# Kernel tuning notes

Hardware: AMD Instinct MI355X
Metric: run time of the kernel (lower is better)

## Reference

```python
import jax, jax.numpy as jnp
import numpy as np

B, S, H, STEPS = 4096, 169, 64, 24  # batch, input seq (window 168 + covariate row), hidden, rollout steps


def _lstm(xseq, Wih, Whh, bih, bhh, h0, c0):
    """PyTorch-style single-layer LSTM. xseq: [B,T,D] -> ([B,T,H], hT, cT). Gate order i,f,g,o."""
    xg = jnp.einsum('btd,gd->btg', xseq, Wih) + (bih + bhh)  # precompute input proj [B,T,4H]

    def step(carry, xg_t):
        h, c = carry
        g = xg_t + h @ Whh.T
        i, f, gg, o = jnp.split(g, 4, axis=-1)
        c = jax.nn.sigmoid(f) * c + jax.nn.sigmoid(i) * jnp.tanh(gg)
        h = jax.nn.sigmoid(o) * jnp.tanh(c)
        return (h, c), h

    (hT, cT), hs = jax.lax.scan(step, (h0, c0), jnp.swapaxes(xg, 0, 1))
    return jnp.swapaxes(hs, 0, 1), hT, cT


def reference(x, Wih1, Whh1, bih1, bhh1, Wih2, Whh2, bih2, bhh2, fc1_w, fc1_b, fc2_w, fc2_b):
    win, d = x[:, :-1, :], x[:, -1, :]  # [B,168,1], [B,1]
    z = jnp.zeros((x.shape[0], H), x.dtype)

    def outer(win, _):
        h1s, h1, c1 = _lstm(win, Wih1, Whh1, bih1, bhh1, z, z)
        h1s = jax.nn.relu(h1s)
        # lstm2 is seeded with lstm1's final (h, c) state, as in the torch code
        h2s, _, _ = _lstm(h1s, Wih2, Whh2, bih2, bhh2, h1, c1)
        feat = jnp.concatenate([jax.nn.relu(h2s[:, -1, :]), d], axis=1)  # [B,65]
        out = (feat @ fc1_w.T + fc1_b) @ fc2_w.T + fc2_b  # [B,1] (no relu between fc1/fc2)
        win = jnp.concatenate([win[:, 1:, :], out[:, :, None]], axis=1)  # slide window
        return win, out[:, 0]

    _, outs = jax.lax.scan(outer, win, None, length=STEPS)  # outs: [24,B]
    return jnp.swapaxes(outs, 0, 1)  # [B,24]


def setup_inputs() -> dict:
    key = jax.random.key(0)
    ks = jax.random.split(key, 14)
    bnd = 1.0 / np.sqrt(H)

    def u(k, shape):
        return jax.random.uniform(k, shape, jnp.float32, -bnd, bnd)

    return {
        'x': jax.random.normal(ks[0], (B, S, 1), jnp.float32),
        'Wih1': u(ks[1], (4 * H, 1)),
        'Whh1': u(ks[2], (4 * H, H)),
        'bih1': u(ks[3], (4 * H,)),
        'bhh1': u(ks[4], (4 * H,)),
        'Wih2': u(ks[5], (4 * H, H)),
        'Whh2': u(ks[6], (4 * H, H)),
        'bih2': u(ks[7], (4 * H,)),
        'bhh2': u(ks[8], (4 * H,)),
        'fc1_w': u(ks[9], (64, 65)),
        'fc1_b': u(ks[10], (64,)),
        'fc2_w': u(ks[11], (1, 64)),
        'fc2_b': u(ks[12], (1,)),
    }
```

## Files before the change

kernel.cpp:

```cpp
#include <hip/hip_runtime.h>
#include <stdint.h>

#define NB 16
#define WIN 168
#define NSTEPS 24
#define NBLK (4096/NB)

typedef __attribute__((ext_vector_type(8))) short bf16x8;
typedef __attribute__((ext_vector_type(4))) float f32x4;

#if __has_builtin(__builtin_amdgcn_rcpf)
#define RCPF(x) __builtin_amdgcn_rcpf(x)
#else
#define RCPF(x) (1.0f / (x))
#endif
#if __has_builtin(__builtin_amdgcn_exp2f)
#define EXP2F(x) __builtin_amdgcn_exp2f(x)
#else
#define EXP2F(x) __expf((x) * 0.6931471805599453f)
#endif

__device__ __forceinline__ float sigm(float x){
  return RCPF(1.0f + EXP2F(x * -1.4426950408889634f));
}
__device__ __forceinline__ float tanh_(float x){
  return __builtin_fmaf(2.0f, RCPF(1.0f + EXP2F(x * -2.8853900817779268f)), -1.0f);
}

__device__ __forceinline__ uint32_t bf_rn(float f){
  uint32_t u = __builtin_bit_cast(uint32_t, f);
  return (u + 0x7FFFu + ((u >> 16) & 1u)) >> 16;
}
__device__ __forceinline__ float bf_f(uint32_t s){
  return __builtin_bit_cast(float, s << 16);
}
__device__ __forceinline__ void split_t(float f, uint32_t& hi, uint32_t& lo){
  uint32_t u = __builtin_bit_cast(uint32_t, f);
  hi = u >> 16;
  lo = bf_rn(f - bf_f(hi));
}
__device__ __forceinline__ void split_s(float f, short& hi, short& lo){
  uint32_t h = bf_rn(f);
  hi = (short)h;
  lo = (short)bf_rn(f - bf_f(h));
}
__device__ __forceinline__ f32x4 mfma16(bf16x8 a, bf16x8 b, f32x4 c){
  return __builtin_amdgcn_mfma_f32_16x16x32_bf16(a, b, c, 0, 0, 0);
}

__device__ __forceinline__ void lstm_epi(const f32x4 acc[4], float c[4], float hn[4]){
  #pragma unroll
  for (int r = 0; r < 4; r++){
    float gi = acc[0][r], gf = acc[1][r], gg = acc[2][r], go = acc[3][r];
    float cn = __builtin_fmaf(sigm(gf), c[r], sigm(gi) * tanh_(gg));
    c[r] = cn;
    hn[r] = sigm(go) * tanh_(cn);
  }
}

#define FROW 136
#define FBLK 544
#define FB(buf,hl,kt) ((((buf)*2 + (hl))*2 + (kt)) * FBLK)
#define BUF_INTS (2*FBLK)

template<bool USE_WS>
__global__ __launch_bounds__(256, 1) void lstm_rec_kernel(
  const float* __restrict__ x,    const float* __restrict__ Wih1, const float* __restrict__ Whh1,
  const float* __restrict__ bih1, const float* __restrict__ bhh1,
  const float* __restrict__ Wih2, const float* __restrict__ Whh2,
  const float* __restrict__ bih2, const float* __restrict__ bhh2,
  const float* __restrict__ fc1w, const float* __restrict__ fc1b,
  const float* __restrict__ fc2w, const float* __restrict__ fc2b,
  float* __restrict__ out, short* __restrict__ hist)
{
  __shared__ __align__(16) short h1f[2*2*2*FBLK];
  __shared__ __align__(16) short r1f[USE_WS ? 16 : 2*2*2*FBLK];
  __shared__ __align__(16) short rlf[USE_WS ? 16 : 2*2*2*FBLK];
  __shared__ float win_s[WIN][NB];
  __shared__ float Hlast[NB][68];
  __shared__ float fc1w_s[64*68];
  __shared__ float dval_s[NB];

  const int tid = threadIdx.x;
  const int wv  = tid >> 6;
  const int ln  = tid & 63;
  const int q   = ln >> 4;
  const int n   = ln & 15;
  const int bg0 = blockIdx.x * NB;
  const int u0  = 16*wv + 4*q;
  const int kt_  = u0 >> 5;
  const int q2_  = (u0 >> 3) & 3;
  const int jj0_ = u0 & 7;
  const int rdo  = q*FROW + n*8;
  const int wro  = q2_*FROW + n*8 + jj0_;
  const int gwo  = kt_*512 + q2_*128 + n*8 + jj0_;
  short* __restrict__ hblk = USE_WS ? (hist + (size_t)blockIdx.x * WIN * 2048) : nullptr;

  for (int i = tid; i < WIN*NB; i += 256){ int t = i >> 4, b = i & 15; win_s[t][b] = x[(bg0 + b)*169 + t]; }
  for (int i = tid; i < 64*65; i += 256){ int j = i / 65, k = i % 65; fc1w_s[j*68 + k] = fc1w[i]; }
  if (tid < NB) dval_s[tid] = x[(bg0 + tid)*169 + 168];

  const float fc1b_r = fc1b[ln];
  const float fc2w_r = fc2w[ln];
  const float fc2b_r = fc2b[0];

  bf16x8 A1hi[4][2], A1lo[4][2], Ain1[4];
  bf16x8 A2hi[4][4], A2lo[4][4];
  f32x4 b1c[4], b2c[4];
  #pragma unroll
  for (int e = 0; e < 4; e++){
    const int ja = 64*e + 16*wv + n;
    #pragma unroll
    for (int kt = 0; kt < 2; kt++){
      const float* p = Whh1 + ja*64 + kt*32 + q*8;
      #pragma unroll
      for (int jj = 0; jj < 8; jj++){ short h,l; split_s(p[jj], h, l); A1hi[e][kt][jj] = h; A1lo[e][kt][jj] = l; }
    }
    #pragma unroll
    for (int kt = 0; kt < 4; kt++){
      const float* p = (kt < 2 ? (Wih2 + ja*64 + kt*32) : (Whh2 + ja*64 + (kt-2)*32)) + q*8;
      #pragma unroll
      for (int jj = 0; jj < 8; jj++){ short h,l; split_s(p[jj], h, l); A2hi[e][kt][jj] = h; A2lo[e][kt][jj] = l; }
    }
    bf16x8 ain = {0,0,0,0,0,0,0,0};
    if (q == 0){ short wh, wl; split_s(Wih1[ja], wh, wl); ain[0] = wh; ain[1] = wh; ain[2] = wl; }
    Ain1[e] = ain;
    const int jc = 64*e + u0;
    #pragma unroll
    for (int r = 0; r < 4; r++){
      b1c[e][r] = bih1[jc+r] + bhh1[jc+r];
      b2c[e][r] = bih2[jc+r] + bhh2[jc+r];
    }
  }

  float c1[4], c2[4], c1r[4];

  auto lstm1_step = [&](short* S, float* cst, int rb, int wb, int slot, int relu_dst, int t){
    bf16x8 Bh0 = *(const bf16x8*)&S[FB(rb,0,0)+rdo];
    bf16x8 Bl0 = *(const bf16x8*)&S[FB(rb,1,0)+rdo];
    bf16x8 Bh1 = *(const bf16x8*)&S[FB(rb,0,1)+rdo];
    bf16x8 Bl1 = *(const bf16x8*)&S[FB(rb,1,1)+rdo];
    bf16x8 bin = {0,0,0,0,0,0,0,0};
    { float xv = win_s[slot][n]; uint32_t xh, xl; split_t(xv, xh, xl);
      if (q == 0){ bin[0] = (short)xh; bin[1] = (short)xl; bin[2] = (short)xh; } }
    f32x4 acc[4];
    #pragma unroll
    for (int e = 0; e < 4; e++){
      f32x4 a = b1c[e];
      a = mfma16(A1hi[e][0], Bh0, a);
      a = mfma16(A1hi[e][0], Bl0, a);
      a = mfma16(A1lo[e][0], Bh0, a);
      a = mfma16(A1hi[e][1], Bh1, a);
      a = mfma16(A1hi[e][1], Bl1, a);
      a = mfma16(A1lo[e][1], Bh1, a);
      a = mfma16(Ain1[e], bin, a);
      acc[e] = a;
    }
    float hn[4];
    lstm_epi(acc, cst, hn);
    uint32_t ph[4], pl[4];
    #pragma unroll
    for (int r = 0; r < 4; r++) split_t(hn[r], ph[r], pl[r]);
    *(uint2*)&S[FB(wb,0,kt_)+wro] = make_uint2(ph[0] | (ph[1]<<16), ph[2] | (ph[3]<<16));
    *(uint2*)&S[FB(wb,1,kt_)+wro] = make_uint2(pl[0] | (pl[1]<<16), pl[2] | (pl[3]<<16));
    if (relu_dst){
      uint32_t sh[4], sl[4];
      #pragma unroll
      for (int r = 0; r < 4; r++){ bool pos = hn[r] > 0.0f; sh[r] = pos ? ph[r] : 0u; sl[r] = pos ? pl[r] : 0u; }
      uint2 phi = make_uint2(sh[0] | (sh[1]<<16), sh[2] | (sh[3]<<16));
      uint2 plo = make_uint2(sl[0] | (sl[1]<<16), sl[2] | (sl[3]<<16));
      if (relu_dst == 1){
        short* Hp = hblk + (size_t)t * 2048;
        *(uint2*)&Hp[gwo]        = phi;
        *(uint2*)&Hp[1024 + gwo] = plo;
      } else {
        *(uint2*)&rlf[FB(rb,0,kt_)+wro] = phi;
        *(uint2*)&rlf[FB(rb,1,kt_)+wro] = plo;
      }
    }
  };

  auto lstm2_core = [&](bf16x8 L1h0, bf16x8 L1l0, bf16x8 L1h1, bf16x8 L1l1, int rbuf, int wbuf, bool last){
    bf16x8 L2h0 = *(const bf16x8*)&h1f[FB(rbuf,0,0)+rdo];
    bf16x8 L2l0 = *(const bf16x8*)&h1f[FB(rbuf,1,0)+rdo];
    bf16x8 L2h1 = *(const bf16x8*)&h1f[FB(rbuf,0,1)+rdo];
    bf16x8 L2l1 = *(const bf16x8*)&h1f[FB(rbuf,1,1)+rdo];
    f32x4 acc[4];
    #pragma unroll
    for (int e = 0; e < 4; e++){
      f32x4 a = b2c[e];
      a = mfma16(A2hi[e][0], L1h0, a);
      a = mfma16(A2hi[e][0], L1l0, a);
      a = mfma16(A2lo[e][0], L1h0, a);
      a = mfma16(A2hi[e][1], L1h1, a);
      a = mfma16(A2hi[e][1], L1l1, a);
      a = mfma16(A2lo[e][1], L1h1, a);
      a = mfma16(A2hi[e][2], L2h0, a);
      a = mfma16(A2hi[e][2], L2l0, a);
      a = mfma16(A2lo[e][2], L2h0, a);
      a = mfma16(A2hi[e][3], L2h1, a);
      a = mfma16(A2hi[e][3], L2l1, a);
      a = mfma16(A2lo[e][3], L2h1, a);
      acc[e] = a;
    }
    float hn[4];
    lstm_epi(acc, c2, hn);
    if (!last){
      uint32_t ph[4], pl[4];
      #pragma unroll
      for (int r = 0; r < 4; r++) split_t(hn[r], ph[r], pl[r]);
      *(uint2*)&h1f[FB(wbuf,0,kt_)+wro] = make_uint2(ph[0] | (ph[1]<<16), ph[2] | (ph[3]<<16));
      *(uint2*)&h1f[FB(wbuf,1,kt_)+wro] = make_uint2(pl[0] | (pl[1]<<16), pl[2] | (pl[3]<<16));
    } else {
      #pragma unroll
      for (int r = 0; r < 4; r++) Hlast[n][u0 + r] = fmaxf(hn[r], 0.0f);
    }
  };

  for (int s = 0; s < NSTEPS; s++){
    { int* p = (int*)&h1f[0];
      for (int i = tid; i < BUF_INTS; i += 256) p[i] = 0; }
    #pragma unroll
    for (int r = 0; r < 4; r++) c1[r] = 0.0f;

    int slot = s;
    for (int t = 0; t < WIN; t++){
      __syncthreads();
      lstm1_step(h1f, c1, t & 1, (t & 1) ^ 1, slot, USE_WS ? 1 : 0, t);
      slot++; if (slot == WIN) slot = 0;
    }

    #pragma unroll
    for (int r = 0; r < 4; r++) c2[r] = c1[r];

    if constexpr (USE_WS) {
      const int ro = q*128 + n*8;
      bf16x8 ch0 = *(const bf16x8*)&hblk[ro];
      bf16x8 cl0 = *(const bf16x8*)&hblk[1024 + ro];
      bf16x8 ch1 = *(const bf16x8*)&hblk[512 + ro];
      bf16x8 cl1 = *(const bf16x8*)&hblk[1536 + ro];
      for (int t = 0; t < WIN; t++){
        bf16x8 nh0, nl0, nh1, nl1;
        if (t < WIN-1){
          const short* Hp = hblk + (size_t)(t+1) * 2048;
          nh0 = *(const bf16x8*)&Hp[ro];
          nl0 = *(const bf16x8*)&Hp[1024 + ro];
          nh1 = *(const bf16x8*)&Hp[512 + ro];
          nl1 = *(const bf16x8*)&Hp[1536 + ro];
        }
        __syncthreads();
        lstm2_core(ch0, cl0, ch1, cl1, t & 1, (t & 1) ^ 1, t == WIN-1);
        ch0 = nh0; cl0 = nl0; ch1 = nh1; cl1 = nl1;
      }
    } else {
      #pragma unroll
      for (int r = 0; r < 4; r++) c1r[r] = 0.0f;
      { int* p = (int*)&r1f[0];
        for (int i = tid; i < BUF_INTS; i += 256) p[i] = 0; }
      slot = s;
      __syncthreads();
      lstm1_step(r1f, c1r, 0, 1, slot, 2, 0);
      slot++;
      for (int i = 1; i < WIN; i++){
        __syncthreads();
        const int rb = i & 1, wb = rb ^ 1;
        lstm1_step(r1f, c1r, rb, wb, slot, 2, i);
        bf16x8 L1h0 = *(const bf16x8*)&rlf[FB(wb,0,0)+rdo];
        bf16x8 L1l0 = *(const bf16x8*)&rlf[FB(wb,1,0)+rdo];
        bf16x8 L1h1 = *(const bf16x8*)&rlf[FB(wb,0,1)+rdo];
        bf16x8 L1l1 = *(const bf16x8*)&rlf[FB(wb,1,1)+rdo];
        lstm2_core(L1h0, L1l0, L1h1, L1l1, wb, rb, false);
        slot++; if (slot == WIN) slot = 0;
      }
      __syncthreads();
      {
        const int rb = (WIN - 1) & 1;
        bf16x8 L1h0 = *(const bf16x8*)&rlf[FB(rb,0,0)+rdo];
        bf16x8 L1l0 = *(const bf16x8*)&rlf[FB(rb,1,0)+rdo];
        bf16x8 L1h1 = *(const bf16x8*)&rlf[FB(rb,0,1)+rdo];
        bf16x8 L1l1 = *(const bf16x8*)&rlf[FB(rb,1,1)+rdo];
        lstm2_core(L1h0, L1l0, L1h1, L1l1, rb, 0, true);
      }
    }
    __syncthreads();

    float o4[4];
    #pragma unroll
    for (int bi = 0; bi < 4; bi++){
      const int b = 4*wv + bi;
      float a1 = fc1b_r;
      #pragma unroll
      for (int k4 = 0; k4 < 16; k4++){
        const float* wp = &fc1w_s[ln*68 + k4*4];
        const float* hp = &Hlast[b][k4*4];
        a1 += wp[0]*hp[0] + wp[1]*hp[1] + wp[2]*hp[2] + wp[3]*hp[3];
      }
      a1 += dval_s[b] * fc1w_s[ln*68 + 64];
      float v = a1 * fc2w_r;
      #pragma unroll
      for (int off = 32; off > 0; off >>= 1) v += __shfl_xor(v, off);
      o4[bi] = v + fc2b_r;
    }
    if (ln == 0){
      #pragma unroll
      for (int bi = 0; bi < 4; bi++){
        const int b = 4*wv + bi;
        out[(bg0 + b)*24 + s] = o4[bi];
        win_s[s % WIN][b] = o4[bi];
      }
    }
  }
}

extern "C" void kernel_launch(void* const* d_in, const int* in_sizes, int n_in,
                              void* d_out, int out_size, void* d_ws, size_t ws_size,
                              hipStream_t stream) {
  (void)in_sizes; (void)n_in; (void)out_size;
  const size_t need = (size_t)NBLK * WIN * 2048 * sizeof(short);
  if (ws_size >= need){
    lstm_rec_kernel<true><<<dim3(NBLK), dim3(256), 0, stream>>>(
        (const float*)d_in[0], (const float*)d_in[1], (const float*)d_in[2],
        (const float*)d_in[3], (const float*)d_in[4], (const float*)d_in[5],
        (const float*)d_in[6], (const float*)d_in[7], (const float*)d_in[8],
        (const float*)d_in[9], (const float*)d_in[10], (const float*)d_in[11],
        (const float*)d_in[12], (float*)d_out, (short*)d_ws);
  } else {
    lstm_rec_kernel<false><<<dim3(NBLK), dim3(256), 0, stream>>>(
        (const float*)d_in[0], (const float*)d_in[1], (const float*)d_in[2],
        (const float*)d_in[3], (const float*)d_in[4], (const float*)d_in[5],
        (const float*)d_in[6], (const float*)d_in[7], (const float*)d_in[8],
        (const float*)d_in[9], (const float*)d_in[10], (const float*)d_in[11],
        (const float*)d_in[12], (float*)d_out, (short*)nullptr);
  }
}
```

Before: 5.761 ms.

## Overlap next rollout step's LSTM1 with current step's LSTM2 in fused loop

In the workspace path, the LSTM1 pass for rollout step sg now runs interleaved with the LSTM2 pass of step sg-1 inside one time loop. LSTM2 reads LSTM1's history from global memory, and its seed state comes from LSTM1's final h in shared memory. The final LSTM1 step is deferred until after the FC head, because it needs the newly predicted window value. This halves the number of serial barrier-separated time loops and lets the two independent MFMA chains fill each other's latency. It also skips the recurrent matmuls on the first step, where h is zero. The cost is extra shared buffers and careful buffer aliasing, so there is a risk of subtle read/write hazards in the history workspace, which is rewritten while being read.

```diff
diff --git a/kernel.cpp b/kernel.cpp
--- a/kernel.cpp
+++ b/kernel.cpp
@@ -63,7 +63,7 @@
 #define FB(buf,hl,kt) ((((buf)*2 + (hl))*2 + (kt)) * FBLK)
 #define BUF_INTS (2*FBLK)
 
-template<bool USE_WS>
+template<bool FUSED>
 __global__ __launch_bounds__(256, 1) void lstm_rec_kernel(
   const float* __restrict__ x,    const float* __restrict__ Wih1, const float* __restrict__ Whh1,
   const float* __restrict__ bih1, const float* __restrict__ bhh1,
@@ -73,9 +73,10 @@
   const float* __restrict__ fc2w, const float* __restrict__ fc2b,
   float* __restrict__ out, short* __restrict__ hist)
 {
-  __shared__ __align__(16) short h1f[2*2*2*FBLK];
-  __shared__ __align__(16) short r1f[USE_WS ? 16 : 2*2*2*FBLK];
-  __shared__ __align__(16) short rlf[USE_WS ? 16 : 2*2*2*FBLK];
+  __shared__ __align__(16) short aS[2*2*2*FBLK];
+  __shared__ __align__(16) short bS[FUSED ? 2*2*2*FBLK : 16];
+  __shared__ __align__(16) short r1f[FUSED ? 16 : 2*2*2*FBLK];
+  __shared__ __align__(16) short rlf[FUSED ? 16 : 2*2*2*FBLK];
   __shared__ float win_s[WIN][NB];
   __shared__ float Hlast[NB][68];
   __shared__ float fc1w_s[64*68];
@@ -94,7 +95,8 @@
   const int rdo  = q*FROW + n*8;
   const int wro  = q2_*FROW + n*8 + jj0_;
   const int gwo  = kt_*512 + q2_*128 + n*8 + jj0_;
-  short* __restrict__ hblk = USE_WS ? (hist + (size_t)blockIdx.x * WIN * 2048) : nullptr;
+  const int ro   = q*128 + n*8;
+  short* __restrict__ hblk = FUSED ? (hist + (size_t)blockIdx.x * WIN * 2048) : nullptr;
 
   for (int i = tid; i < WIN*NB; i += 256){ int t = i >> 4, b = i & 15; win_s[t][b] = x[(bg0 + b)*169 + t]; }
   for (int i = tid; i < 64*65; i += 256){ int j = i / 65, k = i % 65; fc1w_s[j*68 + k] = fc1w[i]; }
@@ -135,26 +137,31 @@
 
   float c1[4], c2[4], c1r[4];
 
-  auto lstm1_step = [&](short* S, float* cst, int rb, int wb, int slot, int relu_dst, int t){
-    bf16x8 Bh0 = *(const bf16x8*)&S[FB(rb,0,0)+rdo];
-    bf16x8 Bl0 = *(const bf16x8*)&S[FB(rb,1,0)+rdo];
-    bf16x8 Bh1 = *(const bf16x8*)&S[FB(rb,0,1)+rdo];
-    bf16x8 Bl1 = *(const bf16x8*)&S[FB(rb,1,1)+rdo];
+  auto lstm1_step = [&](short* S, float* cst, int rb, int wb, int slot, int relu_dst, int t, bool first){
+    f32x4 acc[4];
     bf16x8 bin = {0,0,0,0,0,0,0,0};
     { float xv = win_s[slot][n]; uint32_t xh, xl; split_t(xv, xh, xl);
       if (q == 0){ bin[0] = (short)xh; bin[1] = (short)xl; bin[2] = (short)xh; } }
-    f32x4 acc[4];
-    #pragma unroll
-    for (int e = 0; e < 4; e++){
-      f32x4 a = b1c[e];
-      a = mfma16(A1hi[e][0], Bh0, a);
-      a = mfma16(A1hi[e][0], Bl0, a);
-      a = mfma16(A1lo[e][0], Bh0, a);
-      a = mfma16(A1hi[e][1], Bh1, a);
-      a = mfma16(A1hi[e][1], Bl1, a);
-      a = mfma16(A1lo[e][1], Bh1, a);
-      a = mfma16(Ain1[e], bin, a);
-      acc[e] = a;
+    if (first){
+      #pragma unroll
+      for (int e = 0; e < 4; e++) acc[e] = mfma16(Ain1[e], bin, b1c[e]);
+    } else {
+      bf16x8 Bh0 = *(const bf16x8*)&S[FB(rb,0,0)+rdo];
+      bf16x8 Bl0 = *(const bf16x8*)&S[FB(rb,1,0)+rdo];
+      bf16x8 Bh1 = *(const bf16x8*)&S[FB(rb,0,1)+rdo];
+      bf16x8 Bl1 = *(const bf16x8*)&S[FB(rb,1,1)+rdo];
+      #pragma unroll
+      for (int e = 0; e < 4; e++){
+        f32x4 a = b1c[e];
+        a = mfma16(A1hi[e][0], Bh0, a);
+        a = mfma16(A1hi[e][0], Bl0, a);
+        a = mfma16(A1lo[e][0], Bh0, a);
+        a = mfma16(A1hi[e][1], Bh1, a);
+        a = mfma16(A1hi[e][1], Bl1, a);
+        a = mfma16(A1lo[e][1], Bh1, a);
+        a = mfma16(Ain1[e], bin, a);
+        acc[e] = a;
+      }
     }
     float hn[4];
     lstm_epi(acc, cst, hn);
@@ -180,11 +187,12 @@
     }
   };
 
-  auto lstm2_core = [&](bf16x8 L1h0, bf16x8 L1l0, bf16x8 L1h1, bf16x8 L1l1, int rbuf, int wbuf, bool last){
-    bf16x8 L2h0 = *(const bf16x8*)&h1f[FB(rbuf,0,0)+rdo];
-    bf16x8 L2l0 = *(const bf16x8*)&h1f[FB(rbuf,1,0)+rdo];
-    bf16x8 L2h1 = *(const bf16x8*)&h1f[FB(rbuf,0,1)+rdo];
-    bf16x8 L2l1 = *(const bf16x8*)&h1f[FB(rbuf,1,1)+rdo];
+  auto lstm2_core = [&](bf16x8 L1h0, bf16x8 L1l0, bf16x8 L1h1, bf16x8 L1l1,
+                        const short* Sr, int rbuf, short* Sw, int wbuf, bool last){
+    bf16x8 L2h0 = *(const bf16x8*)&Sr[FB(rbuf,0,0)+rdo];
+    bf16x8 L2l0 = *(const bf16x8*)&Sr[FB(rbuf,1,0)+rdo];
+    bf16x8 L2h1 = *(const bf16x8*)&Sr[FB(rbuf,0,1)+rdo];
+    bf16x8 L2l1 = *(const bf16x8*)&Sr[FB(rbuf,1,1)+rdo];
     f32x4 acc[4];
     #pragma unroll
     for (int e = 0; e < 4; e++){
@@ -209,67 +217,135 @@
       uint32_t ph[4], pl[4];
       #pragma unroll
       for (int r = 0; r < 4; r++) split_t(hn[r], ph[r], pl[r]);
-      *(uint2*)&h1f[FB(wbuf,0,kt_)+wro] = make_uint2(ph[0] | (ph[1]<<16), ph[2] | (ph[3]<<16));
-      *(uint2*)&h1f[FB(wbuf,1,kt_)+wro] = make_uint2(pl[0] | (pl[1]<<16), pl[2] | (pl[3]<<16));
+      *(uint2*)&Sw[FB(wbuf,0,kt_)+wro] = make_uint2(ph[0] | (ph[1]<<16), ph[2] | (ph[3]<<16));
+      *(uint2*)&Sw[FB(wbuf,1,kt_)+wro] = make_uint2(pl[0] | (pl[1]<<16), pl[2] | (pl[3]<<16));
     } else {
       #pragma unroll
       for (int r = 0; r < 4; r++) Hlast[n][u0 + r] = fmaxf(hn[r], 0.0f);
     }
   };
 
-  for (int s = 0; s < NSTEPS; s++){
-    { int* p = (int*)&h1f[0];
-      for (int i = tid; i < BUF_INTS; i += 256) p[i] = 0; }
+  auto hload = [&](int t, bf16x8& h0, bf16x8& l0, bf16x8& h1, bf16x8& l1){
+    const short* Hp = hblk + (size_t)t * 2048;
+    h0 = *(const bf16x8*)&Hp[ro];
+    l0 = *(const bf16x8*)&Hp[1024 + ro];
+    h1 = *(const bf16x8*)&Hp[512 + ro];
+    l1 = *(const bf16x8*)&Hp[1536 + ro];
+  };
+
+  auto fc_head = [&](int s){
+    float o4[4];
+    #pragma unroll
+    for (int bi = 0; bi < 4; bi++){
+      const int b = 4*wv + bi;
+      float a1 = fc1b_r;
+      #pragma unroll
+      for (int k4 = 0; k4 < 16; k4++){
+        const float* wp = &fc1w_s[ln*68 + k4*4];
+        const float* hp = &Hlast[b][k4*4];
+        a1 += wp[0]*hp[0] + wp[1]*hp[1] + wp[2]*hp[2] + wp[3]*hp[3];
+      }
+      a1 += dval_s[b] * fc1w_s[ln*68 + 64];
+      float v = a1 * fc2w_r;
+      #pragma unroll
+      for (int off = 32; off > 0; off >>= 1) v += __shfl_xor(v, off);
+      o4[bi] = v + fc2b_r;
+    }
+    if (ln == 0){
+      #pragma unroll
+      for (int bi = 0; bi < 4; bi++){
+        const int b = 4*wv + bi;
+        out[(bg0 + b)*24 + s] = o4[bi];
+        win_s[s % WIN][b] = o4[bi];
+      }
+    }
+  };
+
+  if constexpr (FUSED){
     #pragma unroll
     for (int r = 0; r < 4; r++) c1[r] = 0.0f;
-
-    int slot = s;
-    for (int t = 0; t < WIN; t++){
-      __syncthreads();
-      lstm1_step(h1f, c1, t & 1, (t & 1) ^ 1, slot, USE_WS ? 1 : 0, t);
+    __syncthreads();
+    lstm1_step(aS, c1, 0, 1, 0, 1, 0, true);
+    for (int t = 1; t < WIN; t++){
+      __syncthreads();
+      lstm1_step(aS, c1, t & 1, (t & 1) ^ 1, t, 1, t, false);
+    }
+
+    for (int sg = 1; sg < NSTEPS; sg++){
+      #pragma unroll
+      for (int r = 0; r < 4; r++){ c2[r] = c1[r]; c1[r] = 0.0f; }
+      bf16x8 ch0, cl0, ch1, cl1, nh0, nl0, nh1, nl1;
+      hload(0, ch0, cl0, ch1, cl1);
+      int slot = sg;
+      hload(1, nh0, nl0, nh1, nl1);
+      __syncthreads();
+      lstm1_step(aS, c1, 0, 1, slot, 1, 0, true);
+      lstm2_core(ch0, cl0, ch1, cl1, aS, 0, bS, 1, false);
+      ch0 = nh0; cl0 = nl0; ch1 = nh1; cl1 = nl1;
       slot++; if (slot == WIN) slot = 0;
+      for (int t = 1; t < WIN-1; t++){
+        hload(t+1, nh0, nl0, nh1, nl1);
+        __syncthreads();
+        lstm1_step(aS, c1, t & 1, (t & 1) ^ 1, slot, 1, t, false);
+        lstm2_core(ch0, cl0, ch1, cl1, bS, t & 1, bS, (t & 1) ^ 1, false);
+        ch0 = nh0; cl0 = nl0; ch1 = nh1; cl1 = nl1;
+        slot++; if (slot == WIN) slot = 0;
+      }
+      __syncthreads();
+      lstm2_core(ch0, cl0, ch1, cl1, bS, 1, bS, 0, true);
+      __syncthreads();
+      fc_head(sg - 1);
+      __syncthreads();
+      lstm1_step(aS, c1, 1, 0, slot, 1, WIN-1, false);
     }
 
     #pragma unroll
     for (int r = 0; r < 4; r++) c2[r] = c1[r];
-
-    if constexpr (USE_WS) {
-      const int ro = q*128 + n*8;
-      bf16x8 ch0 = *(const bf16x8*)&hblk[ro];
-      bf16x8 cl0 = *(const bf16x8*)&hblk[1024 + ro];
-      bf16x8 ch1 = *(const bf16x8*)&hblk[512 + ro];
-      bf16x8 cl1 = *(const bf16x8*)&hblk[1536 + ro];
+    {
+      bf16x8 ch0, cl0, ch1, cl1, nh0, nl0, nh1, nl1;
+      hload(0, ch0, cl0, ch1, cl1);
+      hload(1, nh0, nl0, nh1, nl1);
+      __syncthreads();
+      lstm2_core(ch0, cl0, ch1, cl1, aS, 0, bS, 1, false);
+      ch0 = nh0; cl0 = nl0; ch1 = nh1; cl1 = nl1;
+      for (int t = 1; t < WIN; t++){
+        if (t < WIN-1) hload(t+1, nh0, nl0, nh1, nl1);
+        __syncthreads();
+        lstm2_core(ch0, cl0, ch1, cl1, bS, t & 1, bS, (t & 1) ^ 1, t == WIN-1);
+        ch0 = nh0; cl0 = nl0; ch1 = nh1; cl1 = nl1;
+      }
+      __syncthreads();
+      fc_head(NSTEPS - 1);
+    }
+  } else {
+    for (int s = 0; s < NSTEPS; s++){
+      { int* p = (int*)&aS[0];
+        for (int i = tid; i < BUF_INTS; i += 256) p[i] = 0; }
+      #pragma unroll
+      for (int r = 0; r < 4; r++) c1[r] = 0.0f;
+      int slot = s;
       for (int t = 0; t < WIN; t++){
-        bf16x8 nh0, nl0, nh1, nl1;
-        if (t < WIN-1){
-          const short* Hp = hblk + (size_t)(t+1) * 2048;
-          nh0 = *(const bf16x8*)&Hp[ro];
-          nl0 = *(const bf16x8*)&Hp[1024 + ro];
-          nh1 = *(const bf16x8*)&Hp[512 + ro];
-          nl1 = *(const bf16x8*)&Hp[1536 + ro];
-        }
         __syncthreads();
-        lstm2_core(ch0, cl0, ch1, cl1, t & 1, (t & 1) ^ 1, t == WIN-1);
-        ch0 = nh0; cl0 = nl0; ch1 = nh1; cl1 = nl1;
-      }
-    } else {
-      #pragma unroll
-      for (int r = 0; r < 4; r++) c1r[r] = 0.0f;
+        lstm1_step(aS, c1, t & 1, (t & 1) ^ 1, slot, 0, t, false);
+        slot++; if (slot == WIN) slot = 0;
+      }
+      #pragma unroll
+      for (int r = 0; r < 4; r++){ c2[r] = c1[r]; c1r[r] = 0.0f; }
       { int* p = (int*)&r1f[0];
         for (int i = tid; i < BUF_INTS; i += 256) p[i] = 0; }
       slot = s;
       __syncthreads();
-      lstm1_step(r1f, c1r, 0, 1, slot, 2, 0);
+      lstm1_step(r1f, c1r, 0, 1, slot, 2, 0, false);
       slot++;
       for (int i = 1; i < WIN; i++){
         __syncthreads();
         const int rb = i & 1, wb = rb ^ 1;
-        lstm1_step(r1f, c1r, rb, wb, slot, 2, i);
+        lstm1_step(r1f, c1r, rb, wb, slot, 2, i, false);
         bf16x8 L1h0 = *(const bf16x8*)&rlf[FB(wb,0,0)+rdo];
         bf16x8 L1l0 = *(const bf16x8*)&rlf[FB(wb,1,0)+rdo];
         bf16x8 L1h1 = *(const bf16x8*)&rlf[FB(wb,0,1)+rdo];
         bf16x8 L1l1 = *(const bf16x8*)&rlf[FB(wb,1,1)+rdo];
-        lstm2_core(L1h0, L1l0, L1h1, L1l1, wb, rb, false);
+        lstm2_core(L1h0, L1l0, L1h1, L1l1, aS, wb, aS, rb, false);
         slot++; if (slot == WIN) slot = 0;
       }
       __syncthreads();
@@ -279,35 +355,10 @@
         bf16x8 L1l0 = *(const bf16x8*)&rlf[FB(rb,1,0)+rdo];
         bf16x8 L1h1 = *(const bf16x8*)&rlf[FB(rb,0,1)+rdo];
         bf16x8 L1l1 = *(const bf16x8*)&rlf[FB(rb,1,1)+rdo];
-        lstm2_core(L1h0, L1l0, L1h1, L1l1, rb, 0, true);
-      }
-    }
-    __syncthreads();
-
-    float o4[4];
-    #pragma unroll
-    for (int bi = 0; bi < 4; bi++){
-      const int b = 4*wv + bi;
-      float a1 = fc1b_r;
-      #pragma unroll
-      for (int k4 = 0; k4 < 16; k4++){
-        const float* wp = &fc1w_s[ln*68 + k4*4];
-        const float* hp = &Hlast[b][k4*4];
-        a1 += wp[0]*hp[0] + wp[1]*hp[1] + wp[2]*hp[2] + wp[3]*hp[3];
-      }
-      a1 += dval_s[b] * fc1w_s[ln*68 + 64];
-      float v = a1 * fc2w_r;
-      #pragma unroll
-      for (int off = 32; off > 0; off >>= 1) v += __shfl_xor(v, off);
-      o4[bi] = v + fc2b_r;
-    }
-    if (ln == 0){
-      #pragma unroll
-      for (int bi = 0; bi < 4; bi++){
-        const int b = 4*wv + bi;
-        out[(bg0 + b)*24 + s] = o4[bi];
-        win_s[s % WIN][b] = o4[bi];
-      }
+        lstm2_core(L1h0, L1l0, L1h1, L1l1, aS, rb, aS, 0, true);
+      }
+      __syncthreads();
+      fc_head(s);
     }
   }
 }
```

After: 5.478 ms. -4.9%, faster.
